# Kernel optimization log

Measured on AMD Instinct MI355X. Metric: run time of the kernel, lower is better.

## Reference

```python
import jax, jax.numpy as jnp
import numpy as np

N_NODES = 50000
N_EDGES = 800000
NFEAT = 128
NHID = 128
NCLASS = 10
NUM_GRAPHS = 512


def setup_inputs() -> dict:
    key = jax.random.key(0)
    ks = jax.random.split(key, 12)
    x = jax.random.normal(ks[0], (N_NODES, NFEAT), dtype=jnp.float32)
    edge_index = jax.random.randint(ks[1], (2, N_EDGES), 0, N_NODES, dtype=jnp.int64)
    batch = jnp.sort(jax.random.randint(ks[2], (N_NODES,), 0, NUM_GRAPHS, dtype=jnp.int64))
    def glorot(k, fan_in, fan_out):
        lim = np.sqrt(6.0 / (fan_in + fan_out))
        return jax.random.uniform(k, (fan_in, fan_out), jnp.float32, -lim, lim)
    return {
        "x": x, "edge_index": edge_index, "batch": batch,
        "W0": glorot(ks[3], NFEAT, NHID), "b0": jnp.zeros((NHID,), jnp.float32),
        "W1": glorot(ks[4], NHID, NHID), "b1": jnp.zeros((NHID,), jnp.float32),
        "W2": glorot(ks[5], NHID, NHID), "b2": jnp.zeros((NHID,), jnp.float32),
        "lin_w": glorot(ks[6], NHID, NCLASS), "lin_b": jnp.zeros((NCLASS,), jnp.float32),
    }


def _gcn_norm(edge_index, n):
    # PyG GCNConv: add self-loops, symmetric normalization D^-1/2 A D^-1/2
    loop = jnp.arange(n, dtype=edge_index.dtype)
    src = jnp.concatenate([edge_index[0], loop])  # [E+N]
    dst = jnp.concatenate([edge_index[1], loop])
    deg = jax.ops.segment_sum(jnp.ones_like(dst, dtype=jnp.float32), dst, num_segments=n)
    dis = jnp.where(deg > 0, jax.lax.rsqrt(jnp.maximum(deg, 1.0)), 0.0)
    norm = dis[src] * dis[dst]  # [E+N]
    return src, dst, norm


def _gcn_conv(x, W, b, src, dst, norm, n):
    h = x @ W                              # [N, nhid]
    msg = h[src] * norm[:, None]           # gather + scale, [E+N, nhid]
    out = jax.ops.segment_sum(msg, dst, num_segments=n)
    return out + b


def reference(x, edge_index, batch, W0, b0, W1, b1, W2, b2, lin_w, lin_b):
    n = x.shape[0]
    src, dst, norm = _gcn_norm(edge_index, n)
    h = x
    for (W, b) in ((W0, b0), (W1, b1), (W2, b2)):
        h = jax.nn.relu(_gcn_conv(h, W, b, src, dst, norm, n))
    # global mean pool over graphs
    sums = jax.ops.segment_sum(h, batch, num_segments=NUM_GRAPHS)
    cnts = jax.ops.segment_sum(jnp.ones((n,), jnp.float32), batch, num_segments=NUM_GRAPHS)
    pooled = sums / jnp.maximum(cnts, 1.0)[:, None]  # [G, nhid]
    logits = pooled @ lin_w + lin_b
    return jax.nn.log_softmax(logits, axis=-1)
```

## Files before the change

### kernel.cpp

```cpp
#include <hip/hip_runtime.h>
#include <hip/hip_fp16.h>


#define FEAT 128
#define NCLASS 10
#define NB_MAX 512

typedef _Float16 h8 __attribute__((ext_vector_type(8)));
typedef float f4 __attribute__((ext_vector_type(4)));

__device__ inline float2 h2f2(unsigned u) {
  __half2 h = *reinterpret_cast<__half2*>(&u);
  float2 r;
  r.x = __low2float(h);
  r.y = __high2float(h);
  return r;
}
__device__ inline unsigned f2h2(float a, float b) {
  __half2 h = __floats2half2_rn(a, b);
  return *reinterpret_cast<unsigned*>(&h);
}

__global__ void __launch_bounds__(256) hist_kernel(const int* __restrict__ ei,
                                                   int* __restrict__ bhist,
                                                   int ne, int nb, int epb) {
  __shared__ int lh[NB_MAX];
  int t = threadIdx.x;
  for (int i = t; i < nb; i += 256) lh[i] = 0;
  __syncthreads();
  int r0 = blockIdx.x * epb;
  int r1 = min(r0 + epb, ne);
  for (int k = r0 + t; k < r1; k += 256) atomicAdd(&lh[ei[ne + k] >> 7], 1);
  __syncthreads();
  for (int i = t; i < nb; i += 256)
    if (lh[i]) atomicAdd(&bhist[i], lh[i]);
}

__global__ void __launch_bounds__(512) bscan_kernel(const int* __restrict__ bhist,
                                                    int* __restrict__ bstart,
                                                    int* __restrict__ bcur,
                                                    int* __restrict__ off,
                                                    int nb, int n, int ne) {
  __shared__ int sh[512];
  int t = threadIdx.x;
  int v = (t < nb) ? bhist[t] : 0;
  sh[t] = v;
  __syncthreads();
  int x = v;
  for (int d = 1; d < 512; d <<= 1) {
    int y = (t >= d) ? sh[t - d] : 0;
    __syncthreads();
    x += y;
    sh[t] = x;
    __syncthreads();
  }
  if (t < nb) {
    bstart[t] = x - v;
    bcur[t] = x - v;
  }
  if (t == 0) {
    bstart[nb] = ne;
    off[n] = ne;
  }
}

__global__ void __launch_bounds__(256) scatter_kernel(const int* __restrict__ ei,
                                                      int* __restrict__ bcur,
                                                      unsigned* __restrict__ buf,
                                                      int ne, int nb, int epb) {
  __shared__ int lh[NB_MAX], lbs[NB_MAX];
  int t = threadIdx.x;
  for (int i = t; i < nb; i += 256) lh[i] = 0;
  __syncthreads();
  int r0 = blockIdx.x * epb;
  int r1 = min(r0 + epb, ne);
  for (int k = r0 + t; k < r1; k += 256) atomicAdd(&lh[ei[ne + k] >> 7], 1);
  __syncthreads();
  for (int i = t; i < nb; i += 256) {
    int c = lh[i];
    lbs[i] = c ? atomicAdd(&bcur[i], c) : 0;
    lh[i] = 0;
  }
  __syncthreads();
  for (int k = r0 + t; k < r1; k += 256) {
    int src = ei[k];
    int dst = ei[ne + k];
    int b = dst >> 7;
    int p = lbs[b] + atomicAdd(&lh[b], 1);
    buf[p] = (unsigned)src | ((unsigned)(dst & 127) << 25);
  }
}

__global__ void __launch_bounds__(256) bucket_build_kernel(const unsigned* __restrict__ buf,
                                                           const int* __restrict__ bstart,
                                                           int* __restrict__ off,
                                                           int* __restrict__ csr,
                                                           float* __restrict__ dis, int n) {
  __shared__ int cnt[128], cur[128], sh[128];
  int b = blockIdx.x, t = threadIdx.x;
  int e0 = bstart[b], e1 = bstart[b + 1];
  if (t < 128) cnt[t] = 0;
  __syncthreads();
  for (int k = e0 + t; k < e1; k += 256) atomicAdd(&cnt[buf[k] >> 25], 1);
  __syncthreads();
  int v = (t < 128) ? cnt[t] : 0;
  if (t < 128) sh[t] = v;
  __syncthreads();
  int x = v;
  for (int d = 1; d < 128; d <<= 1) {
    int y = (t < 128 && t >= d) ? sh[t - d] : 0;
    __syncthreads();
    if (t < 128) {
      x += y;
      sh[t] = x;
    }
    __syncthreads();
  }
  if (t < 128) {
    int node = (b << 7) + t;
    cur[t] = x - v;
    if (node < n) {
      off[node] = e0 + x - v;
      dis[node] = rsqrtf((float)(v + 1));
    }
  }
  __syncthreads();
  for (int k = e0 + t; k < e1; k += 256) {
    unsigned u = buf[k];
    int d = u >> 25;
    int p = atomicAdd(&cur[d], 1);
    csr[e0 + p] = (int)(u & 0x1FFFFFFu);
  }
}

__global__ void wtcvt_kernel(const float* __restrict__ W0, const float* __restrict__ W1,
                             const float* __restrict__ W2, _Float16* __restrict__ Wt) {
  int i = blockIdx.x * 256 + threadIdx.x;
  if (i >= 3 * FEAT * FEAT) return;
  int l = i / (FEAT * FEAT);
  int r = i - l * (FEAT * FEAT);
  int nn = r >> 7, kk = r & 127;
  const float* W = (l == 0) ? W0 : (l == 1) ? W1 : W2;
  Wt[i] = (_Float16)W[kk * FEAT + nn];
}

template <bool F32IN>
__global__ void __launch_bounds__(256) gemm_mfma_kernel(const void* __restrict__ Xin,
                                                        const _Float16* __restrict__ Wt,
                                                        const float* __restrict__ dis,
                                                        _Float16* __restrict__ Hs, int n) {
  __shared__ _Float16 st[64 * FEAT];
  int tid = threadIdx.x;
  int w = tid >> 6, lane = tid & 63;
  int l15 = lane & 15, hi = lane >> 4;

  int rowA = blockIdx.x * 64 + w * 16 + l15;
  int rA = min(rowA, n - 1);
  const _Float16* Xh = (const _Float16*)Xin;
  const float* Xf = (const float*)Xin;

  f4 acc[8];
#pragma unroll
  for (int nb = 0; nb < 8; ++nb) acc[nb] = (f4)(0.f);

#pragma unroll
  for (int kk = 0; kk < FEAT; kk += 32) {
    int ko = kk + hi * 8;
    h8 a;
    if (F32IN) {
      float4 x0 = *(const float4*)&Xf[(size_t)rA * FEAT + ko];
      float4 x1 = *(const float4*)&Xf[(size_t)rA * FEAT + ko + 4];
      a[0] = (_Float16)x0.x; a[1] = (_Float16)x0.y; a[2] = (_Float16)x0.z; a[3] = (_Float16)x0.w;
      a[4] = (_Float16)x1.x; a[5] = (_Float16)x1.y; a[6] = (_Float16)x1.z; a[7] = (_Float16)x1.w;
    } else {
      a = *(const h8*)&Xh[(size_t)rA * FEAT + ko];
    }
#pragma unroll
    for (int nb = 0; nb < 8; ++nb) {
      h8 bfr = *(const h8*)&Wt[(nb * 16 + l15) * FEAT + ko];
      acc[nb] = __builtin_amdgcn_mfma_f32_16x16x32_f16(a, bfr, acc[nb], 0, 0, 0);
    }
  }

  float dv[4];
#pragma unroll
  for (int r = 0; r < 4; ++r) {
    int grow = blockIdx.x * 64 + w * 16 + hi * 4 + r;
    dv[r] = dis[min(grow, n - 1)];
  }
#pragma unroll
  for (int nb = 0; nb < 8; ++nb)
#pragma unroll
    for (int r = 0; r < 4; ++r)
      st[(w * 16 + hi * 4 + r) * FEAT + nb * 16 + l15] = (_Float16)(acc[nb][r] * dv[r]);
  __syncthreads();

  int rowbase = blockIdx.x * 64;
#pragma unroll
  for (int i = tid; i < 64 * FEAT / 8; i += 256) {
    int row = rowbase + (i >> 4);
    if (row < n)
      *(uint4*)&Hs[(size_t)row * FEAT + (i & 15) * 8] =
          *(const uint4*)&st[(i >> 4) * FEAT + (i & 15) * 8];
  }
}

__global__ void __launch_bounds__(256) agg_kernel(const unsigned* __restrict__ Hs,
                                                  const int* __restrict__ csr,
                                                  const int* __restrict__ off,
                                                  const float* __restrict__ dis,
                                                  const float* __restrict__ b,
                                                  unsigned* __restrict__ out, int n) {
  int wave = threadIdx.x >> 6;
  int lane = threadIdx.x & 63;
  int node = blockIdx.x * 4 + wave;
  if (node >= n) return;
  int s = off[node];
  int e = off[node + 1];
  float2 a0 = h2f2(Hs[node * 64 + lane]);
  float2 a1 = make_float2(0.f, 0.f), a2 = make_float2(0.f, 0.f), a3 = make_float2(0.f, 0.f);
  float2 a4 = make_float2(0.f, 0.f), a5 = make_float2(0.f, 0.f);
  float2 a6 = make_float2(0.f, 0.f), a7 = make_float2(0.f, 0.f);
  int k = s;
  for (; k + 8 <= e; k += 8) {
    int s0 = csr[k], s1 = csr[k + 1], s2 = csr[k + 2], s3 = csr[k + 3];
    int s4 = csr[k + 4], s5 = csr[k + 5], s6 = csr[k + 6], s7 = csr[k + 7];
    unsigned u0 = Hs[s0 * 64 + lane], u1 = Hs[s1 * 64 + lane];
    unsigned u2 = Hs[s2 * 64 + lane], u3 = Hs[s3 * 64 + lane];
    unsigned u4 = Hs[s4 * 64 + lane], u5 = Hs[s5 * 64 + lane];
    unsigned u6 = Hs[s6 * 64 + lane], u7 = Hs[s7 * 64 + lane];
    float2 v0 = h2f2(u0), v1 = h2f2(u1), v2 = h2f2(u2), v3 = h2f2(u3);
    float2 v4 = h2f2(u4), v5 = h2f2(u5), v6 = h2f2(u6), v7 = h2f2(u7);
    a0.x += v0.x; a0.y += v0.y;
    a1.x += v1.x; a1.y += v1.y;
    a2.x += v2.x; a2.y += v2.y;
    a3.x += v3.x; a3.y += v3.y;
    a4.x += v4.x; a4.y += v4.y;
    a5.x += v5.x; a5.y += v5.y;
    a6.x += v6.x; a6.y += v6.y;
    a7.x += v7.x; a7.y += v7.y;
  }
  for (; k + 4 <= e; k += 4) {
    int s0 = csr[k], s1 = csr[k + 1], s2 = csr[k + 2], s3 = csr[k + 3];
    unsigned u0 = Hs[s0 * 64 + lane], u1 = Hs[s1 * 64 + lane];
    unsigned u2 = Hs[s2 * 64 + lane], u3 = Hs[s3 * 64 + lane];
    float2 v0 = h2f2(u0), v1 = h2f2(u1), v2 = h2f2(u2), v3 = h2f2(u3);
    a0.x += v0.x; a0.y += v0.y;
    a1.x += v1.x; a1.y += v1.y;
    a2.x += v2.x; a2.y += v2.y;
    a3.x += v3.x; a3.y += v3.y;
  }
  for (; k < e; ++k) {
    float2 v = h2f2(Hs[csr[k] * 64 + lane]);
    a0.x += v.x;
    a0.y += v.y;
  }
  a0.x += a1.x + a2.x + a3.x + a4.x + a5.x + a6.x + a7.x;
  a0.y += a1.y + a2.y + a3.y + a4.y + a5.y + a6.y + a7.y;
  float d = dis[node];
  float2 bb = ((const float2*)b)[lane];
  float ox = fmaxf(fmaf(d, a0.x, bb.x), 0.f);
  float oy = fmaxf(fmaf(d, a0.y, bb.y), 0.f);
  out[node * 64 + lane] = f2h2(ox, oy);
}

__global__ void bounds_kernel(const int* __restrict__ batch, int* __restrict__ gstart,
                              int n, int g) {
  int i = blockIdx.x * 256 + threadIdx.x;
  if (i >= n) return;
  int bi = batch[i];
  int bp = (i == 0) ? -1 : batch[i - 1];
  for (int q = bp + 1; q <= bi; ++q) gstart[q] = i;
  if (i == n - 1) {
    for (int q = bi + 1; q <= g; ++q) gstart[q] = n;
  }
}

__global__ void __launch_bounds__(128) pool_kernel(const __half* __restrict__ h,
                                                   const int* __restrict__ gstart,
                                                   const float* __restrict__ lw,
                                                   const float* __restrict__ lb,
                                                   float* __restrict__ out) {
  int g = blockIdx.x;
  int t = threadIdx.x;
  int s = gstart[g];
  int e = gstart[g + 1];
  float a0 = 0.f, a1 = 0.f, a2 = 0.f, a3 = 0.f;
  int i = s;
  for (; i + 4 <= e; i += 4) {
    a0 += __half2float(h[(size_t)i * FEAT + t]);
    a1 += __half2float(h[(size_t)(i + 1) * FEAT + t]);
    a2 += __half2float(h[(size_t)(i + 2) * FEAT + t]);
    a3 += __half2float(h[(size_t)(i + 3) * FEAT + t]);
  }
  for (; i < e; ++i) a0 += __half2float(h[(size_t)i * FEAT + t]);
  float acc = a0 + a1 + a2 + a3;
  float cnt = (float)(e - s);
  float pooled = acc / fmaxf(cnt, 1.f);
  __shared__ float lds[FEAT];
  __shared__ float logits[NCLASS];
  lds[t] = pooled;
  __syncthreads();
  if (t < NCLASS) {
    float z = lb[t];
    for (int k = 0; k < FEAT; ++k) z += lds[k] * lw[k * NCLASS + t];
    logits[t] = z;
  }
  __syncthreads();
  if (t < NCLASS) {
    float m = logits[0];
#pragma unroll
    for (int c = 1; c < NCLASS; ++c) m = fmaxf(m, logits[c]);
    float ssum = 0.f;
#pragma unroll
    for (int c = 0; c < NCLASS; ++c) ssum += expf(logits[c] - m);
    out[(size_t)g * NCLASS + t] = logits[t] - m - logf(ssum);
  }
}

extern "C" void kernel_launch(void* const* d_in, const int* in_sizes, int n_in,
                              void* d_out, int out_size, void* d_ws, size_t ws_size,
                              hipStream_t stream) {
  const float* x = (const float*)d_in[0];
  const int* ei = (const int*)d_in[1];
  const int* batch = (const int*)d_in[2];
  const float* W0 = (const float*)d_in[3];
  const float* b0 = (const float*)d_in[4];
  const float* W1 = (const float*)d_in[5];
  const float* b1 = (const float*)d_in[6];
  const float* W2 = (const float*)d_in[7];
  const float* b2 = (const float*)d_in[8];
  const float* lw = (const float*)d_in[9];
  const float* lb = (const float*)d_in[10];

  int n = in_sizes[2];
  int ne = in_sizes[1] / 2;
  int g = out_size / NCLASS;
  int nb = (n + 127) >> 7;
  int hblocks = 120;
  int epb = (ne + hblocks - 1) / hblocks;

  char* ws = (char*)d_ws;
  size_t p = 0;
  auto alloc = [&](size_t bytes) {
    size_t cur = p;
    p += (bytes + 255) & ~(size_t)255;
    return cur;
  };
  int* off = (int*)(ws + alloc((size_t)(n + 1) * 4));
  int* csr = (int*)(ws + alloc((size_t)ne * 4));
  int* bhist = (int*)(ws + alloc((size_t)NB_MAX * 4));
  int* bstart = (int*)(ws + alloc((size_t)(NB_MAX + 1) * 4));
  int* bcur = (int*)(ws + alloc((size_t)NB_MAX * 4));
  int* gstart = (int*)(ws + alloc((size_t)(g + 1) * 4));
  float* dis = (float*)(ws + alloc((size_t)n * 4));
  unsigned* buf = (unsigned*)(ws + alloc((size_t)ne * 4));
  _Float16* Wt = (_Float16*)(ws + alloc((size_t)3 * FEAT * FEAT * 2));
  _Float16* Hs = (_Float16*)(ws + alloc((size_t)n * FEAT * 2));
  _Float16* Hb = (_Float16*)(ws + alloc((size_t)n * FEAT * 2));

  hipMemsetAsync(bhist, 0, NB_MAX * 4, stream);

  hist_kernel<<<hblocks, 256, 0, stream>>>(ei, bhist, ne, nb, epb);
  bscan_kernel<<<1, 512, 0, stream>>>(bhist, bstart, bcur, off, nb, n, ne);
  scatter_kernel<<<hblocks, 256, 0, stream>>>(ei, bcur, buf, ne, nb, epb);
  bucket_build_kernel<<<nb, 256, 0, stream>>>(buf, bstart, off, csr, dis, n);
  wtcvt_kernel<<<(3 * FEAT * FEAT + 255) / 256, 256, 0, stream>>>(W0, W1, W2, Wt);

  const float* bv[3] = {b0, b1, b2};
  for (int l = 0; l < 3; ++l) {
    const void* in = (l == 0) ? (const void*)x : (const void*)Hb;
    const _Float16* wt = Wt + (size_t)l * FEAT * FEAT;
    if (l == 0)
      gemm_mfma_kernel<true><<<(n + 63) / 64, 256, 0, stream>>>(in, wt, dis, Hs, n);
    else
      gemm_mfma_kernel<false><<<(n + 63) / 64, 256, 0, stream>>>(in, wt, dis, Hs, n);
    agg_kernel<<<(n + 3) / 4, 256, 0, stream>>>((const unsigned*)Hs, csr, off, dis, bv[l],
                                                (unsigned*)Hb, n);
  }

  bounds_kernel<<<(n + 255) / 256, 256, 0, stream>>>(batch, gstart, n, g);
  pool_kernel<<<g, 128, 0, stream>>>((const __half*)Hb, gstart, lw, lb, (float*)d_out);
}
```

Measured before the change: 233.9 us.

## Vectorize aggregation gathers to 16-byte rows with 4 edges per wave

Rewrites the GCN aggregation so each wave splits into four 16-lane groups. Each lane loads 8 halves (16 bytes) of a neighbor row, the groups handle different edges in parallel, and the partial sums are combined with cross-lane shuffles. The aim is fewer, wider memory requests and more edges in flight per wave. It also merges the weight-conversion kernel into the histogram kernel as extra blocks, saving one launch. The costs are predicated tail loads, shuffle reductions, and only a quarter of the lanes writing output.

```diff
diff --git a/kernel.cpp b/kernel.cpp
--- a/kernel.cpp
+++ b/kernel.cpp
@@ -9,23 +9,26 @@
 typedef _Float16 h8 __attribute__((ext_vector_type(8)));
 typedef float f4 __attribute__((ext_vector_type(4)));
 
-__device__ inline float2 h2f2(unsigned u) {
-  __half2 h = *reinterpret_cast<__half2*>(&u);
-  float2 r;
-  r.x = __low2float(h);
-  r.y = __high2float(h);
-  return r;
-}
-__device__ inline unsigned f2h2(float a, float b) {
-  __half2 h = __floats2half2_rn(a, b);
-  return *reinterpret_cast<unsigned*>(&h);
-}
-
-__global__ void __launch_bounds__(256) hist_kernel(const int* __restrict__ ei,
-                                                   int* __restrict__ bhist,
-                                                   int ne, int nb, int epb) {
+__global__ void __launch_bounds__(256) hist_wt_kernel(const int* __restrict__ ei,
+                                                      int* __restrict__ bhist,
+                                                      int ne, int nb, int epb, int hb,
+                                                      const float* __restrict__ W0,
+                                                      const float* __restrict__ W1,
+                                                      const float* __restrict__ W2,
+                                                      _Float16* __restrict__ Wt) {
+  int t = threadIdx.x;
+  if (blockIdx.x >= hb) {
+    int i = (blockIdx.x - hb) * 256 + t;
+    if (i < 3 * FEAT * FEAT) {
+      int l = i / (FEAT * FEAT);
+      int r = i - l * (FEAT * FEAT);
+      int nn = r >> 7, kk = r & 127;
+      const float* W = (l == 0) ? W0 : (l == 1) ? W1 : W2;
+      Wt[i] = (_Float16)W[kk * FEAT + nn];
+    }
+    return;
+  }
   __shared__ int lh[NB_MAX];
-  int t = threadIdx.x;
   for (int i = t; i < nb; i += 256) lh[i] = 0;
   __syncthreads();
   int r0 = blockIdx.x * epb;
@@ -131,17 +134,6 @@
     int p = atomicAdd(&cur[d], 1);
     csr[e0 + p] = (int)(u & 0x1FFFFFFu);
   }
-}
-
-__global__ void wtcvt_kernel(const float* __restrict__ W0, const float* __restrict__ W1,
-                             const float* __restrict__ W2, _Float16* __restrict__ Wt) {
-  int i = blockIdx.x * 256 + threadIdx.x;
-  if (i >= 3 * FEAT * FEAT) return;
-  int l = i / (FEAT * FEAT);
-  int r = i - l * (FEAT * FEAT);
-  int nn = r >> 7, kk = r & 127;
-  const float* W = (l == 0) ? W0 : (l == 1) ? W1 : W2;
-  Wt[i] = (_Float16)W[kk * FEAT + nn];
 }
 
 template <bool F32IN>
@@ -205,63 +197,79 @@
   }
 }
 
-__global__ void __launch_bounds__(256) agg_kernel(const unsigned* __restrict__ Hs,
+__global__ void __launch_bounds__(256) agg_kernel(const h8* __restrict__ Hs,
                                                   const int* __restrict__ csr,
                                                   const int* __restrict__ off,
                                                   const float* __restrict__ dis,
                                                   const float* __restrict__ b,
-                                                  unsigned* __restrict__ out, int n) {
+                                                  h8* __restrict__ out, int n) {
   int wave = threadIdx.x >> 6;
   int lane = threadIdx.x & 63;
+  int grp = lane >> 4, lig = lane & 15;
   int node = blockIdx.x * 4 + wave;
   if (node >= n) return;
   int s = off[node];
   int e = off[node + 1];
-  float2 a0 = h2f2(Hs[node * 64 + lane]);
-  float2 a1 = make_float2(0.f, 0.f), a2 = make_float2(0.f, 0.f), a3 = make_float2(0.f, 0.f);
-  float2 a4 = make_float2(0.f, 0.f), a5 = make_float2(0.f, 0.f);
-  float2 a6 = make_float2(0.f, 0.f), a7 = make_float2(0.f, 0.f);
-  int k = s;
-  for (; k + 8 <= e; k += 8) {
-    int s0 = csr[k], s1 = csr[k + 1], s2 = csr[k + 2], s3 = csr[k + 3];
-    int s4 = csr[k + 4], s5 = csr[k + 5], s6 = csr[k + 6], s7 = csr[k + 7];
-    unsigned u0 = Hs[s0 * 64 + lane], u1 = Hs[s1 * 64 + lane];
-    unsigned u2 = Hs[s2 * 64 + lane], u3 = Hs[s3 * 64 + lane];
-    unsigned u4 = Hs[s4 * 64 + lane], u5 = Hs[s5 * 64 + lane];
-    unsigned u6 = Hs[s6 * 64 + lane], u7 = Hs[s7 * 64 + lane];
-    float2 v0 = h2f2(u0), v1 = h2f2(u1), v2 = h2f2(u2), v3 = h2f2(u3);
-    float2 v4 = h2f2(u4), v5 = h2f2(u5), v6 = h2f2(u6), v7 = h2f2(u7);
-    a0.x += v0.x; a0.y += v0.y;
-    a1.x += v1.x; a1.y += v1.y;
-    a2.x += v2.x; a2.y += v2.y;
-    a3.x += v3.x; a3.y += v3.y;
-    a4.x += v4.x; a4.y += v4.y;
-    a5.x += v5.x; a5.y += v5.y;
-    a6.x += v6.x; a6.y += v6.y;
-    a7.x += v7.x; a7.y += v7.y;
-  }
-  for (; k + 4 <= e; k += 4) {
-    int s0 = csr[k], s1 = csr[k + 1], s2 = csr[k + 2], s3 = csr[k + 3];
-    unsigned u0 = Hs[s0 * 64 + lane], u1 = Hs[s1 * 64 + lane];
-    unsigned u2 = Hs[s2 * 64 + lane], u3 = Hs[s3 * 64 + lane];
-    float2 v0 = h2f2(u0), v1 = h2f2(u1), v2 = h2f2(u2), v3 = h2f2(u3);
-    a0.x += v0.x; a0.y += v0.y;
-    a1.x += v1.x; a1.y += v1.y;
-    a2.x += v2.x; a2.y += v2.y;
-    a3.x += v3.x; a3.y += v3.y;
-  }
-  for (; k < e; ++k) {
-    float2 v = h2f2(Hs[csr[k] * 64 + lane]);
-    a0.x += v.x;
-    a0.y += v.y;
-  }
-  a0.x += a1.x + a2.x + a3.x + a4.x + a5.x + a6.x + a7.x;
-  a0.y += a1.y + a2.y + a3.y + a4.y + a5.y + a6.y + a7.y;
-  float d = dis[node];
-  float2 bb = ((const float2*)b)[lane];
-  float ox = fmaxf(fmaf(d, a0.x, bb.x), 0.f);
-  float oy = fmaxf(fmaf(d, a0.y, bb.y), 0.f);
-  out[node * 64 + lane] = f2h2(ox, oy);
+
+  float acc[8];
+  if (grp == 0) {
+    h8 v = Hs[(size_t)node * 16 + lig];
+#pragma unroll
+    for (int j = 0; j < 8; ++j) acc[j] = (float)v[j];
+  } else {
+#pragma unroll
+    for (int j = 0; j < 8; ++j) acc[j] = 0.f;
+  }
+
+  for (int k = s; k < e; k += 16) {
+    int k0 = k + grp, k1 = k0 + 4, k2 = k0 + 8, k3 = k0 + 12;
+    int i0 = (k0 < e) ? csr[k0] : -1;
+    int i1 = (k1 < e) ? csr[k1] : -1;
+    int i2 = (k2 < e) ? csr[k2] : -1;
+    int i3 = (k3 < e) ? csr[k3] : -1;
+    h8 v0 = Hs[(size_t)max(i0, 0) * 16 + lig];
+    h8 v1 = Hs[(size_t)max(i1, 0) * 16 + lig];
+    h8 v2 = Hs[(size_t)max(i2, 0) * 16 + lig];
+    h8 v3 = Hs[(size_t)max(i3, 0) * 16 + lig];
+    if (i0 >= 0) {
+#pragma unroll
+      for (int j = 0; j < 8; ++j) acc[j] += (float)v0[j];
+    }
+    if (i1 >= 0) {
+#pragma unroll
+      for (int j = 0; j < 8; ++j) acc[j] += (float)v1[j];
+    }
+    if (i2 >= 0) {
+#pragma unroll
+      for (int j = 0; j < 8; ++j) acc[j] += (float)v2[j];
+    }
+    if (i3 >= 0) {
+#pragma unroll
+      for (int j = 0; j < 8; ++j) acc[j] += (float)v3[j];
+    }
+  }
+
+#pragma unroll
+  for (int j = 0; j < 8; ++j) {
+    acc[j] += __shfl_xor(acc[j], 16);
+    acc[j] += __shfl_xor(acc[j], 32);
+  }
+
+  if (grp == 0) {
+    float d = dis[node];
+    float4 b0 = ((const float4*)b)[lig * 2];
+    float4 b1 = ((const float4*)b)[lig * 2 + 1];
+    h8 o;
+    o[0] = (_Float16)fmaxf(fmaf(d, acc[0], b0.x), 0.f);
+    o[1] = (_Float16)fmaxf(fmaf(d, acc[1], b0.y), 0.f);
+    o[2] = (_Float16)fmaxf(fmaf(d, acc[2], b0.z), 0.f);
+    o[3] = (_Float16)fmaxf(fmaf(d, acc[3], b0.w), 0.f);
+    o[4] = (_Float16)fmaxf(fmaf(d, acc[4], b1.x), 0.f);
+    o[5] = (_Float16)fmaxf(fmaf(d, acc[5], b1.y), 0.f);
+    o[6] = (_Float16)fmaxf(fmaf(d, acc[6], b1.z), 0.f);
+    o[7] = (_Float16)fmaxf(fmaf(d, acc[7], b1.w), 0.f);
+    out[(size_t)node * 16 + lig] = o;
+  }
 }
 
 __global__ void bounds_kernel(const int* __restrict__ batch, int* __restrict__ gstart,
@@ -339,6 +347,7 @@
   int nb = (n + 127) >> 7;
   int hblocks = 120;
   int epb = (ne + hblocks - 1) / hblocks;
+  int wtblocks = (3 * FEAT * FEAT + 255) / 256;
 
   char* ws = (char*)d_ws;
   size_t p = 0;
@@ -361,11 +370,11 @@
 
   hipMemsetAsync(bhist, 0, NB_MAX * 4, stream);
 
-  hist_kernel<<<hblocks, 256, 0, stream>>>(ei, bhist, ne, nb, epb);
+  hist_wt_kernel<<<hblocks + wtblocks, 256, 0, stream>>>(ei, bhist, ne, nb, epb, hblocks,
+                                                         W0, W1, W2, Wt);
   bscan_kernel<<<1, 512, 0, stream>>>(bhist, bstart, bcur, off, nb, n, ne);
   scatter_kernel<<<hblocks, 256, 0, stream>>>(ei, bcur, buf, ne, nb, epb);
   bucket_build_kernel<<<nb, 256, 0, stream>>>(buf, bstart, off, csr, dis, n);
-  wtcvt_kernel<<<(3 * FEAT * FEAT + 255) / 256, 256, 0, stream>>>(W0, W1, W2, Wt);
 
   const float* bv[3] = {b0, b1, b2};
   for (int l = 0; l < 3; ++l) {
@@ -375,8 +384,8 @@
       gemm_mfma_kernel<true><<<(n + 63) / 64, 256, 0, stream>>>(in, wt, dis, Hs, n);
     else
       gemm_mfma_kernel<false><<<(n + 63) / 64, 256, 0, stream>>>(in, wt, dis, Hs, n);
-    agg_kernel<<<(n + 3) / 4, 256, 0, stream>>>((const unsigned*)Hs, csr, off, dis, bv[l],
-                                                (unsigned*)Hb, n);
+    agg_kernel<<<(n + 3) / 4, 256, 0, stream>>>((const h8*)Hs, csr, off, dis, bv[l],
+                                                (h8*)Hb, n);
   }
 
   bounds_kernel<<<(n + 255) / 256, 256, 0, stream>>>(batch, gstart, n, g);
```

Result: faster. 222.5 us (-4.9%).
